# Kernel tuning notes

Measured on AMD Instinct MI355X. Metric: run time of the kernel, lower is better.

## Reference

```python
import jax, jax.numpy as jnp
import numpy as np

M, N, DIM = 256, 256, 512
NUM_EPOCHS = 100
ALPHA = 0.3
SIGMA = max(M, N) / 2.0


def _neuron_locations(m, n):
    ii, jj = jnp.meshgrid(jnp.arange(m), jnp.arange(n), indexing='ij')
    return jnp.stack([ii.reshape(-1), jj.reshape(-1)], axis=1)  # [m*n, 2] int32


def setup_inputs() -> dict:
    key = jax.random.key(0)
    k1, k2 = jax.random.split(key)
    input_vector = jax.random.normal(k1, (DIM,), dtype=jnp.float32)
    weights = jax.random.normal(k2, (M * N, DIM), dtype=jnp.float32)
    epoch = 10
    return {"input_vector": input_vector, "weights": weights, "epoch": epoch}


def reference(input_vector, weights, epoch):
    locs = _neuron_locations(M, N)  # [m*n, 2]
    # --- BMU search: broadcast distance + argmin (no tiling needed) ---
    diff = weights - input_vector[None, :]                  # [m*n, dim]
    distance = jnp.sqrt(jnp.sum(diff * diff, axis=1))       # [m*n]
    bmu_index = jnp.argmin(distance)
    bmu_loc = locs[bmu_index]                               # [2]
    # --- training update ---
    epoch_f = jnp.float32(epoch)
    learning_rate = 1.0 - epoch_f / NUM_EPOCHS
    alpha_op = ALPHA * learning_rate
    sigma_op = SIGMA * learning_rate
    loc_diff = locs - bmu_loc[None, :]                      # [m*n, 2]
    bmu_dist_sq = jnp.sum(loc_diff * loc_diff, axis=1).astype(jnp.float32)  # [m*n]
    neighbourhood = jnp.exp(-bmu_dist_sq / (sigma_op * sigma_op))
    lr_mult = (alpha_op * neighbourhood)[:, None]           # [m*n, 1]
    new_weights = weights + lr_mult * (input_vector[None, :] - weights)
    return bmu_loc, new_weights
```

## Files before the change

### kernel.cpp

```cpp
#include <hip/hip_runtime.h>

#define SOM_M 256
#define SOM_N 256
#define SOM_DIM 512
#define SOM_ROWS (SOM_M * SOM_N)
#define SOM_ELEMS (SOM_ROWS * SOM_DIM)

__global__ __launch_bounds__(256) void som_bmu_partial(
    const float* __restrict__ w, const float* __restrict__ in,
    float* __restrict__ pd, int* __restrict__ pi) {
  __shared__ float s_in[SOM_DIM];
  for (int i = threadIdx.x; i < SOM_DIM; i += blockDim.x) s_in[i] = in[i];
  __syncthreads();

  const int wave = threadIdx.x >> 6;
  const int lane = threadIdx.x & 63;
  const int wavesPerBlock = blockDim.x >> 6;
  const int globalWave = blockIdx.x * wavesPerBlock + wave;
  const int nWaves = gridDim.x * wavesPerBlock;

  float best = 3.4e38f;
  int bestIdx = 0x7FFFFFFF;

  const float4* in4 = (const float4*)s_in;
  for (int row = globalWave; row < SOM_ROWS; row += nWaves) {
    const float4* wr = (const float4*)(w + (size_t)row * SOM_DIM);
    float acc = 0.f;
#pragma unroll
    for (int k = 0; k < 2; ++k) {
      float4 wv = wr[lane + 64 * k];
      float4 iv = in4[lane + 64 * k];
      float dx = wv.x - iv.x;
      float dy = wv.y - iv.y;
      float dz = wv.z - iv.z;
      float dw = wv.w - iv.w;
      acc += dx * dx + dy * dy + dz * dz + dw * dw;
    }
#pragma unroll
    for (int off = 32; off; off >>= 1) acc += __shfl_xor(acc, off, 64);
    if (acc < best) { best = acc; bestIdx = row; }
  }

  __shared__ float sb[8];
  __shared__ int si[8];
  if (lane == 0) { sb[wave] = best; si[wave] = bestIdx; }
  __syncthreads();
  if (threadIdx.x == 0) {
    float b = sb[0];
    int bi = si[0];
    for (int k = 1; k < wavesPerBlock; ++k) {
      if (sb[k] < b || (sb[k] == b && si[k] < bi)) { b = sb[k]; bi = si[k]; }
    }
    pd[blockIdx.x] = b;
    pi[blockIdx.x] = bi;
  }
}

__global__ __launch_bounds__(256) void som_bmu_final(
    const float* __restrict__ pd, const int* __restrict__ pi, int nb,
    float* __restrict__ out, int* __restrict__ bmu) {
  float best = 3.4e38f;
  int bi = 0x7FFFFFFF;
  for (int i = threadIdx.x; i < nb; i += blockDim.x) {
    float d = pd[i];
    int idx = pi[i];
    if (d < best || (d == best && idx < bi)) { best = d; bi = idx; }
  }
  __shared__ float sd[256];
  __shared__ int sx[256];
  sd[threadIdx.x] = best;
  sx[threadIdx.x] = bi;
  __syncthreads();
  for (int s = 128; s; s >>= 1) {
    if ((int)threadIdx.x < s) {
      float od = sd[threadIdx.x + s];
      int ox = sx[threadIdx.x + s];
      if (od < sd[threadIdx.x] || (od == sd[threadIdx.x] && ox < sx[threadIdx.x])) {
        sd[threadIdx.x] = od;
        sx[threadIdx.x] = ox;
      }
    }
    __syncthreads();
  }
  if (threadIdx.x == 0) {
    int idx = sx[0];
    int r = idx >> 8;
    int c = idx & 255;
    out[0] = (float)r;
    out[1] = (float)c;
    bmu[0] = r;
    bmu[1] = c;
  }
}

__global__ __launch_bounds__(256) void som_update(
    const float* __restrict__ w, const float* __restrict__ in,
    const int* __restrict__ epoch_p, const int* __restrict__ bmu,
    float* __restrict__ out_w ) {
  const float lr = 1.0f - (float)epoch_p[0] / 100.0f;
  const float alpha_op = 0.3f * lr;
  const float sigma_op = 128.0f * lr;
  const float inv_s2 = 1.0f / (sigma_op * sigma_op);
  const int br = bmu[0];
  const int bc = bmu[1];

  const float4* w4 = (const float4*)w;
  const float4* in4 = (const float4*)in;
  float2* o2 = (float2*)out_w;

  const int total4 = SOM_ELEMS / 4;
  const int stride = gridDim.x * blockDim.x;
  for (int i = blockIdx.x * blockDim.x + threadIdx.x; i < total4; i += stride) {
    const int elem = i << 2;
    const int row = elem >> 9;
    const int c4 = (elem & 511) >> 2;
    const int rr = (row >> 8) - br;
    const int cc = (row & 255) - bc;
    const float d2 = (float)(rr * rr + cc * cc);
    const float mult = alpha_op * __expf(-d2 * inv_s2);

    float4 wv = w4[i];
    float4 iv = in4[c4];
    float2 a, b;
    a.x = wv.x + mult * (iv.x - wv.x);
    a.y = wv.y + mult * (iv.y - wv.y);
    b.x = wv.z + mult * (iv.z - wv.z);
    b.y = wv.w + mult * (iv.w - wv.w);
    o2[2 * i] = a;
    o2[2 * i + 1] = b;
  }
}

extern "C" void kernel_launch(void* const* d_in, const int* in_sizes, int n_in,
                              void* d_out, int out_size, void* d_ws, size_t ws_size,
                              hipStream_t stream) {
  const float* input_vector = (const float*)d_in[0];
  const float* weights = (const float*)d_in[1];
  const int* epoch = (const int*)d_in[2];
  float* out = (float*)d_out;

  const int NB = 2048;
  float* pd = (float*)d_ws;
  int* pi = (int*)((char*)d_ws + NB * 4);
  int* bmu = (int*)((char*)d_ws + 2 * NB * 4);

  som_bmu_partial<<<NB, 256, 0, stream>>>(weights, input_vector, pd, pi);
  som_bmu_final<<<1, 256, 0, stream>>>(pd, pi, NB, out, bmu);
  som_update<<<2048, 256, 0, stream>>>(weights, input_vector, epoch, bmu, out + 2);
}
```

Baseline: 73.66 us.

## Replace two-stage BMU reduction with packed 64-bit atomicMin and nontemporal stores

Packs each candidate's non-negative float distance and row index into one 64-bit key so a single global atomicMin picks the BMU. This removes the separate single-block final-reduction kernel and its launch, adding a small memset instead. The update kernel now decodes the BMU itself and writes the location outputs. Output stores use nontemporal hints to reduce cache pollution, and element-wise maths uses ext_vector types.

```diff
diff --git a/kernel.cpp b/kernel.cpp
--- a/kernel.cpp
+++ b/kernel.cpp
@@ -6,107 +6,77 @@
 #define SOM_ROWS (SOM_M * SOM_N)
 #define SOM_ELEMS (SOM_ROWS * SOM_DIM)
 
-__global__ __launch_bounds__(256) void som_bmu_partial(
+typedef float f32x4 __attribute__((ext_vector_type(4)));
+typedef float f32x2 __attribute__((ext_vector_type(2)));
+
+__global__ __launch_bounds__(256) void som_bmu(
     const float* __restrict__ w, const float* __restrict__ in,
-    float* __restrict__ pd, int* __restrict__ pi) {
+    unsigned long long* __restrict__ best) {
   __shared__ float s_in[SOM_DIM];
-  for (int i = threadIdx.x; i < SOM_DIM; i += blockDim.x) s_in[i] = in[i];
+  for (int i = threadIdx.x; i < SOM_DIM; i += 256) s_in[i] = in[i];
   __syncthreads();
 
   const int wave = threadIdx.x >> 6;
   const int lane = threadIdx.x & 63;
-  const int wavesPerBlock = blockDim.x >> 6;
-  const int globalWave = blockIdx.x * wavesPerBlock + wave;
-  const int nWaves = gridDim.x * wavesPerBlock;
+  const int globalWave = blockIdx.x * 4 + wave;
+  const int nWaves = gridDim.x * 4;
 
-  float best = 3.4e38f;
-  int bestIdx = 0x7FFFFFFF;
+  float bd = 3.4e38f;
+  int bi = SOM_ROWS;
 
-  const float4* in4 = (const float4*)s_in;
+  const f32x4* in4 = (const f32x4*)s_in;
   for (int row = globalWave; row < SOM_ROWS; row += nWaves) {
-    const float4* wr = (const float4*)(w + (size_t)row * SOM_DIM);
+    const f32x4* wr = (const f32x4*)(w + (size_t)row * SOM_DIM);
     float acc = 0.f;
 #pragma unroll
     for (int k = 0; k < 2; ++k) {
-      float4 wv = wr[lane + 64 * k];
-      float4 iv = in4[lane + 64 * k];
-      float dx = wv.x - iv.x;
-      float dy = wv.y - iv.y;
-      float dz = wv.z - iv.z;
-      float dw = wv.w - iv.w;
-      acc += dx * dx + dy * dy + dz * dz + dw * dw;
+      f32x4 wv = wr[lane + 64 * k];
+      f32x4 iv = in4[lane + 64 * k];
+      f32x4 d = wv - iv;
+      acc += d.x * d.x + d.y * d.y + d.z * d.z + d.w * d.w;
     }
 #pragma unroll
     for (int off = 32; off; off >>= 1) acc += __shfl_xor(acc, off, 64);
-    if (acc < best) { best = acc; bestIdx = row; }
+    if (acc < bd) { bd = acc; bi = row; }
   }
 
-  __shared__ float sb[8];
-  __shared__ int si[8];
-  if (lane == 0) { sb[wave] = best; si[wave] = bestIdx; }
+  unsigned long long pk =
+      ((unsigned long long)__float_as_uint(bd) << 32) | (unsigned int)bi;
+
+  __shared__ unsigned long long sp[4];
+  if (lane == 0) sp[wave] = pk;
   __syncthreads();
   if (threadIdx.x == 0) {
-    float b = sb[0];
-    int bi = si[0];
-    for (int k = 1; k < wavesPerBlock; ++k) {
-      if (sb[k] < b || (sb[k] == b && si[k] < bi)) { b = sb[k]; bi = si[k]; }
-    }
-    pd[blockIdx.x] = b;
-    pi[blockIdx.x] = bi;
-  }
-}
-
-__global__ __launch_bounds__(256) void som_bmu_final(
-    const float* __restrict__ pd, const int* __restrict__ pi, int nb,
-    float* __restrict__ out, int* __restrict__ bmu) {
-  float best = 3.4e38f;
-  int bi = 0x7FFFFFFF;
-  for (int i = threadIdx.x; i < nb; i += blockDim.x) {
-    float d = pd[i];
-    int idx = pi[i];
-    if (d < best || (d == best && idx < bi)) { best = d; bi = idx; }
-  }
-  __shared__ float sd[256];
-  __shared__ int sx[256];
-  sd[threadIdx.x] = best;
-  sx[threadIdx.x] = bi;
-  __syncthreads();
-  for (int s = 128; s; s >>= 1) {
-    if ((int)threadIdx.x < s) {
-      float od = sd[threadIdx.x + s];
-      int ox = sx[threadIdx.x + s];
-      if (od < sd[threadIdx.x] || (od == sd[threadIdx.x] && ox < sx[threadIdx.x])) {
-        sd[threadIdx.x] = od;
-        sx[threadIdx.x] = ox;
-      }
-    }
-    __syncthreads();
-  }
-  if (threadIdx.x == 0) {
-    int idx = sx[0];
-    int r = idx >> 8;
-    int c = idx & 255;
-    out[0] = (float)r;
-    out[1] = (float)c;
-    bmu[0] = r;
-    bmu[1] = c;
+    unsigned long long m = sp[0];
+#pragma unroll
+    for (int k = 1; k < 4; ++k) m = (sp[k] < m) ? sp[k] : m;
+    atomicMin(best, m);
   }
 }
 
 __global__ __launch_bounds__(256) void som_update(
     const float* __restrict__ w, const float* __restrict__ in,
-    const int* __restrict__ epoch_p, const int* __restrict__ bmu,
-    float* __restrict__ out_w ) {
+    const int* __restrict__ epoch_p,
+    const unsigned long long* __restrict__ best,
+    float* __restrict__ out ) {
+  const unsigned long long pk = *best;
+  const int bidx = (int)(unsigned int)(pk & 0xFFFFFFFFull);
+  const int br = bidx >> 8;
+  const int bc = bidx & 255;
+
+  if (blockIdx.x == 0 && threadIdx.x == 0) {
+    out[0] = (float)br;
+    out[1] = (float)bc;
+  }
+
   const float lr = 1.0f - (float)epoch_p[0] / 100.0f;
   const float alpha_op = 0.3f * lr;
   const float sigma_op = 128.0f * lr;
   const float inv_s2 = 1.0f / (sigma_op * sigma_op);
-  const int br = bmu[0];
-  const int bc = bmu[1];
 
-  const float4* w4 = (const float4*)w;
-  const float4* in4 = (const float4*)in;
-  float2* o2 = (float2*)out_w;
+  const f32x4* w4 = (const f32x4*)w;
+  const f32x4* in4 = (const f32x4*)in;
+  f32x2* o2 = (f32x2*)(out + 2);
 
   const int total4 = SOM_ELEMS / 4;
   const int stride = gridDim.x * blockDim.x;
@@ -119,15 +89,13 @@
     const float d2 = (float)(rr * rr + cc * cc);
     const float mult = alpha_op * __expf(-d2 * inv_s2);
 
-    float4 wv = w4[i];
-    float4 iv = in4[c4];
-    float2 a, b;
-    a.x = wv.x + mult * (iv.x - wv.x);
-    a.y = wv.y + mult * (iv.y - wv.y);
-    b.x = wv.z + mult * (iv.z - wv.z);
-    b.y = wv.w + mult * (iv.w - wv.w);
-    o2[2 * i] = a;
-    o2[2 * i + 1] = b;
+    f32x4 wv = w4[i];
+    f32x4 iv = in4[c4];
+    f32x4 r = wv + mult * (iv - wv);
+    f32x2 a; a.x = r.x; a.y = r.y;
+    f32x2 b; b.x = r.z; b.y = r.w;
+    __builtin_nontemporal_store(a, &o2[2 * i]);
+    __builtin_nontemporal_store(b, &o2[2 * i + 1]);
   }
 }
 
@@ -139,12 +107,9 @@
   const int* epoch = (const int*)d_in[2];
   float* out = (float*)d_out;
 
-  const int NB = 2048;
-  float* pd = (float*)d_ws;
-  int* pi = (int*)((char*)d_ws + NB * 4);
-  int* bmu = (int*)((char*)d_ws + 2 * NB * 4);
+  unsigned long long* best = (unsigned long long*)d_ws;
 
-  som_bmu_partial<<<NB, 256, 0, stream>>>(weights, input_vector, pd, pi);
-  som_bmu_final<<<1, 256, 0, stream>>>(pd, pi, NB, out, bmu);
-  som_update<<<2048, 256, 0, stream>>>(weights, input_vector, epoch, bmu, out + 2);
+  hipMemsetAsync(best, 0xFF, 8, stream);
+  som_bmu<<<2048, 256, 0, stream>>>(weights, input_vector, best);
+  som_update<<<2048, 256, 0, stream>>>(weights, input_vector, epoch, best, out);
 }
```

Measured after the change: 92.00 us. 24.9% more time.
